# Optimization experiments

Measured on AMD Instinct MI355X. Metric: run time of the kernel, lower is better.

## Reference

```python
import jax, jax.numpy as jnp
import numpy as np

# model dims (DeepSeekV2-Lite-like, reduced expert count)
H = 2048      # hidden_dim
NH = 16       # num_heads
NOPE = 128    # qk_nope_head_dim
ROPE = 64     # qk_rope_head_dim (interleaved rotary)
VD = 128      # v_head_dim
QL = 1536     # q_lora_rank
KVL = 512     # kv_lora_rank
E = 8         # num routed experts
TOPK = 2      # num_experts_per_token
MI = 512      # moe_intermediate_dim
SH_I = 2 * MI # num_shared_experts * moe_intermediate_dim
B = 1
S = 2048
T = B * S
EPS = 1e-6
MOE_SCALE = 1.0  # gating_scaling_factor


def setup_inputs() -> dict:
    key = jax.random.key(0)
    ks = jax.random.split(key, 16)
    def w(k, shape):
        return jax.random.normal(k, shape, dtype=jnp.float32) * 0.02
    # interleaved rotary tables: one angle per (even,odd) pair
    half = ROPE // 2
    pos = jnp.arange(S, dtype=jnp.float32)
    inv_freq = 1.0 / (10000.0 ** (jnp.arange(half, dtype=jnp.float32) * 2.0 / ROPE))
    ang = pos[:, None] * inv_freq[None, :]              # [S, half]
    sin = jnp.tile(jnp.sin(ang), (B, 1))                # [T, half]
    cos = jnp.tile(jnp.cos(ang), (B, 1))
    return {
        "x": jax.random.normal(ks[0], (T, H), jnp.float32),
        "skip": jax.random.normal(ks[1], (T, H), jnp.float32),
        "rotary_sin": sin,
        "rotary_cos": cos,
        "ln1_w": jnp.ones((H,), jnp.float32),
        "ln2_w": jnp.ones((H,), jnp.float32),
        "w_qa": w(ks[2], (QL, H)),
        "qa_norm_w": jnp.ones((QL,), jnp.float32),
        "w_qb": w(ks[3], (NH * (NOPE + ROPE), QL)),
        "w_kva": w(ks[4], (KVL + ROPE, H)),
        "kva_norm_w": jnp.ones((KVL,), jnp.float32),
        "w_kb": w(ks[5], (NH * NOPE, KVL)),
        "w_vb": w(ks[6], (NH * VD, KVL)),
        "w_o": w(ks[7], (H, NH * VD)),
        "gate_w": w(ks[8], (E, H)),
        "moe_up_w": w(ks[9], (E, 2 * MI, H)),
        "moe_down_w": w(ks[10], (E, H, MI)),
        "shared_up_w": w(ks[11], (2 * SH_I, H)),
        "shared_down_w": w(ks[12], (H, SH_I)),
        "batch": B,
    }


def _rms(v, w):
    return v * jax.lax.rsqrt(jnp.mean(v * v, axis=-1, keepdims=True) + EPS) * w


def _rope_interleaved(v, sin, cos):
    # v: [T, nh, ROPE]; sin/cos: [T, ROPE//2]; rotate (even, odd) pairs
    x1, x2 = v[..., 0::2], v[..., 1::2]
    s, c = sin[:, None, :], cos[:, None, :]
    o1 = x1 * c - x2 * s
    o2 = x1 * s + x2 * c
    return jnp.stack([o1, o2], axis=-1).reshape(v.shape)


def reference(x, skip, rotary_sin, rotary_cos, ln1_w, ln2_w, w_qa, qa_norm_w,
              w_qb, w_kva, kva_norm_w, w_kb, w_vb, w_o, gate_w,
              moe_up_w, moe_down_w, shared_up_w, shared_down_w, batch):
    Tt = x.shape[0]
    Sq = Tt // batch
    # SkipRMSNorm #1
    x1 = x + skip
    n1 = _rms(x1, ln1_w)
    # ---- MLA attention (prefill path, decoding_batches=0) ----
    qa = _rms(n1 @ w_qa.T, qa_norm_w)                               # [T, QL]
    q = (qa @ w_qb.T).reshape(Tt, NH, NOPE + ROPE)
    q_nope, q_pe = q[..., :NOPE], q[..., NOPE:]
    q_pe = _rope_interleaved(q_pe, rotary_sin, rotary_cos)
    kv = n1 @ w_kva.T                                               # [T, KVL+ROPE]
    ckv = _rms(kv[:, :KVL], kva_norm_w)
    k_pe = _rope_interleaved(kv[:, KVL:][:, None, :], rotary_sin, rotary_cos)  # [T,1,ROPE]
    k_nope = (ckv @ w_kb.T).reshape(Tt, NH, NOPE)
    v = (ckv @ w_vb.T).reshape(Tt, NH, VD)
    qf = jnp.concatenate([q_nope, q_pe], -1).reshape(batch, Sq, NH, NOPE + ROPE)
    kf = jnp.concatenate([k_nope, jnp.broadcast_to(k_pe, (Tt, NH, ROPE))], -1)
    kf = kf.reshape(batch, Sq, NH, NOPE + ROPE)
    vf = v.reshape(batch, Sq, NH, VD)
    scale = 1.0 / np.sqrt(NOPE + ROPE)
    scores = jnp.einsum('bqhd,bkhd->bhqk', qf, kf) * scale
    causal = jnp.tril(jnp.ones((Sq, Sq), bool))
    scores = jnp.where(causal[None, None], scores, jnp.float32(-1e30))
    p = jax.nn.softmax(scores, axis=-1)
    o = jnp.einsum('bhqk,bkhd->bqhd', p, vf).reshape(Tt, NH * VD)
    attn = o @ w_o.T
    # SkipRMSNorm #2
    x2 = x1 + attn
    n2 = _rms(x2, ln2_w)
    # ---- MoE FFN: softmax gate, greedy top-k, normalized probs ----
    probs = jax.nn.softmax(n2 @ gate_w.T, axis=-1)                  # [T, E]
    tv, ti = jax.lax.top_k(probs, TOPK)
    tv = tv / jnp.sum(tv, axis=-1, keepdims=True) * MOE_SCALE
    routed = jnp.zeros_like(n2)
    for e in range(E):  # fixed small expert count; masked dense dispatch
        we = jnp.sum(tv * (ti == e), axis=-1)                       # [T]
        h = n2 @ moe_up_w[e].T                                      # [T, 2*MI]
        h = jax.nn.silu(h[:, :MI]) * h[:, MI:]
        routed = routed + we[:, None] * (h @ moe_down_w[e].T)
    # shared experts (dense swiglu MLP)
    hs = n2 @ shared_up_w.T
    hs = jax.nn.silu(hs[:, :SH_I]) * hs[:, SH_I:]
    ffn = routed + hs @ shared_down_w.T
    return (x2, ffn)
```

## Files before the change

### kernel.cpp

```cpp
#include <hip/hip_runtime.h>
#include <hip/hip_bf16.h>

#define H 2048
#define NH 16
#define NOPE 128
#define ROPE_D 64
#define DQK 192
#define VD 128
#define QL 1536
#define KVL 512
#define NE 8
#define MI_D 512
#define SHI 1024
#define EPS 1e-6f
#define MAXA 5120

typedef unsigned short bfu;
typedef short bf16x8 __attribute__((ext_vector_type(8)));
typedef float f32x4 __attribute__((ext_vector_type(4)));

#define MFMA16(a, b, c) __builtin_amdgcn_mfma_f32_16x16x32_bf16(a, b, c, 0, 0, 0)

#define BAR_PLAIN()   asm volatile("s_barrier" ::: "memory")
#define BAR_LGKM0()   asm volatile("s_waitcnt lgkmcnt(0)\n\ts_barrier" ::: "memory")
#define BAR_VM4()     asm volatile("s_waitcnt vmcnt(4)\n\ts_barrier" ::: "memory")
#define BAR_VM0()     asm volatile("s_waitcnt vmcnt(0)\n\ts_barrier" ::: "memory")

__device__ __forceinline__ float bf2f(bfu u) {
    union { unsigned int i; float f; } w; w.i = ((unsigned int)u) << 16; return w.f;
}
__device__ __forceinline__ bfu f2bf(float f) {
    union { float f; unsigned int i; } u; u.f = f;
    return (bfu)((u.i + 0x7fffu + ((u.i >> 16) & 1u)) >> 16);
}

__device__ __forceinline__ void async16(const bfu* g, bfu* l) {
    __builtin_amdgcn_global_load_lds((const __attribute__((address_space(1))) void*)g,
                                     (__attribute__((address_space(3))) void*)l, 16, 0, 0);
}

__device__ __forceinline__ float blk_sum(float v) {
    __shared__ float sb[4];
    for (int o = 32; o > 0; o >>= 1) v += __shfl_down(v, o, 64);
    int lane = threadIdx.x & 63, w = threadIdx.x >> 6;
    __syncthreads();
    if (lane == 0) sb[w] = v;
    __syncthreads();
    return sb[0] + sb[1] + sb[2] + sb[3];
}

struct GemmSeg {
    const bfu* A; const bfu* B; void* C; void* C2;
    const int* aidx; const int* eid;
    long bstride;
    int N, K, ldm3, mode, nx, ntiles;
};

__device__ __forceinline__ void gemm_body(const bfu* __restrict__ A, const bfu* __restrict__ B,
                                          void* __restrict__ Cv, void* __restrict__ Cv2,
                                          int N, int K, int ldm3, int mode,
                                          const int* __restrict__ aidx,
                                          const int* __restrict__ eid, long bstride,
                                          int bx, int by,
                                          bfu* sAb, bfu* sBb) {
    bfu (*sA)[128 * 32] = (bfu (*)[128 * 32])sAb;
    bfu (*sB)[128 * 32] = (bfu (*)[128 * 32])sBb;
    const int tid = threadIdx.x;
    const int lane = tid & 63, w = tid >> 6;
    const int quad = lane >> 4, li = lane & 15;
    const int m0 = by * 128, n0 = bx * 128;
    const bfu* Bp = B + (eid ? (size_t)eid[by] * bstride : 0);

    const int l4 = lane >> 2;
    const int lg = lane & 3;
    const int kc = lg ^ ((lane >> 3) & 3);
    int r0 = m0 + w * 32 + l4, r1 = r0 + 16;
    if (aidx) { r0 = aidx[r0]; r1 = aidx[r1]; }
    const bfu* gA0 = A + (size_t)r0 * K + kc * 8;
    const bfu* gA1 = A + (size_t)r1 * K + kc * 8;
    const bfu* gB0 = Bp + (size_t)(n0 + w * 32 + l4) * K + kc * 8;
    const bfu* gB1 = gB0 + (size_t)16 * K;
    const int oA0 = (w * 32) * 32, oA1 = (w * 32 + 16) * 32;

    const int wm = (w >> 1) * 64, wn = (w & 1) * 64;
    const int fg = (quad ^ ((li >> 1) & 3)) * 8;
    int oa[4], ob[4];
#pragma unroll
    for (int t4 = 0; t4 < 4; ++t4) {
        oa[t4] = (wm + t4 * 16 + li) * 32 + fg;
        ob[t4] = (wn + t4 * 16 + li) * 32 + fg;
    }
    f32x4 acc[4][4];
#pragma unroll
    for (int i = 0; i < 4; ++i)
#pragma unroll
        for (int j = 0; j < 4; ++j) acc[i][j] = (f32x4){0.f, 0.f, 0.f, 0.f};

    const int nb = K / 32;
    async16(gA0, &sA[0][oA0]); async16(gA1, &sA[0][oA1]);
    async16(gB0, &sB[0][oA0]); async16(gB1, &sB[0][oA1]);
    async16(gA0 + 32, &sA[1][oA0]); async16(gA1 + 32, &sA[1][oA1]);
    async16(gB0 + 32, &sB[1][oA0]); async16(gB1 + 32, &sB[1][oA1]);

    int cur = 0;
    for (int it = 0; it < nb; ++it) {
        if (it < nb - 1) { BAR_VM4(); } else { BAR_VM0(); }
        bf16x8 av[4], bv[4];
#pragma unroll
        for (int t4 = 0; t4 < 4; ++t4) av[t4] = *(const bf16x8*)&sA[cur][oa[t4]];
#pragma unroll
        for (int t4 = 0; t4 < 4; ++t4) bv[t4] = *(const bf16x8*)&sB[cur][ob[t4]];
        if (it + 2 < nb) {
            const int k1 = (it + 2) * 32;
            int nxt = cur + 2; if (nxt >= 3) nxt -= 3;
            async16(gA0 + k1, &sA[nxt][oA0]); async16(gA1 + k1, &sA[nxt][oA1]);
            async16(gB0 + k1, &sB[nxt][oA0]); async16(gB1 + k1, &sB[nxt][oA1]);
        }
#pragma unroll
        for (int mt = 0; mt < 4; ++mt)
#pragma unroll
            for (int nt = 0; nt < 4; ++nt)
                acc[mt][nt] = MFMA16(av[mt], bv[nt], acc[mt][nt]);
        if (++cur >= 3) cur = 0;
    }

#pragma unroll
    for (int mt = 0; mt < 4; ++mt)
#pragma unroll
        for (int nt = 0; nt < 4; ++nt) {
            int row = m0 + wm + mt * 16 + quad * 4;
            int col = n0 + wn + nt * 16 + li;
            if (mode == 0) {
                float* C = (float*)Cv;
#pragma unroll
                for (int r = 0; r < 4; ++r) C[(size_t)(row + r) * N + col] = acc[mt][nt][r];
            } else if (mode == 1) {
                bfu* C = (bfu*)Cv;
#pragma unroll
                for (int r = 0; r < 4; ++r) C[(size_t)(row + r) * N + col] = f2bf(acc[mt][nt][r]);
            } else {
                if (n0 < 2048) {
                    bfu* C = (bfu*)Cv;
#pragma unroll
                    for (int r = 0; r < 4; ++r) C[(size_t)(row + r) * 2048 + col] = f2bf(acc[mt][nt][r]);
                } else {
                    bfu* C2 = (bfu*)Cv2;
                    ushort4 u;
                    u.x = f2bf(acc[mt][nt][0]); u.y = f2bf(acc[mt][nt][1]);
                    u.z = f2bf(acc[mt][nt][2]); u.w = f2bf(acc[mt][nt][3]);
                    *(ushort4*)(C2 + (size_t)(col - 2048) * ldm3 + row) = u;
                }
            }
        }
}

__global__ __launch_bounds__(256) void gemm_multi(GemmSeg s0, GemmSeg s1) {
    __shared__ bfu sA[3][128 * 32];
    __shared__ bfu sB[3][128 * 32];
    int b = blockIdx.x;
    if (b < s0.ntiles) {
        gemm_body(s0.A, s0.B, s0.C, s0.C2, s0.N, s0.K, s0.ldm3, s0.mode,
                  s0.aidx, s0.eid, s0.bstride, b % s0.nx, b / s0.nx, &sA[0][0], &sB[0][0]);
    } else {
        int lb = b - s0.ntiles;
        gemm_body(s1.A, s1.B, s1.C, s1.C2, s1.N, s1.K, s1.ldm3, s1.mode,
                  s1.aidx, s1.eid, s1.bstride, lb % s1.nx, lb / s1.nx, &sA[0][0], &sB[0][0]);
    }
}

struct CastArgs {
    const float* s[10];
    bfu* d[10];
    unsigned start[11];
    int pad[10];
};
__global__ __launch_bounds__(256) void k_cast_all(CastArgs a) {
    unsigned g = blockIdx.x * 256 + threadIdx.x;
    if (g >= a.start[10]) return;
    int id = 0;
#pragma unroll
    for (int i = 1; i < 10; ++i) if (g >= a.start[i]) id = i;
    size_t i8 = (size_t)(g - a.start[id]) * 8;
    ushort4 u0 = {0, 0, 0, 0}, u1 = {0, 0, 0, 0};
    if (!a.pad[id] || (i8 >> 11) < 576) {
        const float* s = a.s[id];
        float4 x0 = *(const float4*)(s + i8);
        float4 x1 = *(const float4*)(s + i8 + 4);
        u0.x = f2bf(x0.x); u0.y = f2bf(x0.y); u0.z = f2bf(x0.z); u0.w = f2bf(x0.w);
        u1.x = f2bf(x1.x); u1.y = f2bf(x1.y); u1.z = f2bf(x1.z); u1.w = f2bf(x1.w);
    }
    bfu* d = a.d[id];
    *(ushort4*)(d + i8) = u0;
    *(ushort4*)(d + i8 + 4) = u1;
}

__global__ __launch_bounds__(256) void k_add_rms(const float* __restrict__ x, const float* __restrict__ skip,
                                                 const float* __restrict__ w,
                                                 float* __restrict__ x1, bfu* __restrict__ n1b) {
    int t = blockIdx.x;
    size_t base = (size_t)t * H;
    float loc[8]; float ss = 0.f;
#pragma unroll
    for (int i = 0; i < 8; ++i) {
        int c = threadIdx.x + i * 256;
        float v = x[base + c] + skip[base + c];
        loc[i] = v; ss += v * v;
        x1[base + c] = v;
    }
    float tot = blk_sum(ss);
    float r = rsqrtf(tot / (float)H + EPS);
#pragma unroll
    for (int i = 0; i < 8; ++i) {
        int c = threadIdx.x + i * 256;
        n1b[base + c] = f2bf(loc[i] * r * w[c]);
    }
}

__global__ __launch_bounds__(256) void k_qkv_post(const bfu* __restrict__ qkv,
                                                  const float* __restrict__ qa_nw,
                                                  const float* __restrict__ kva_nw,
                                                  const float* __restrict__ sin_, const float* __restrict__ cos_,
                                                  bfu* __restrict__ qab, bfu* __restrict__ ckv,
                                                  bfu* __restrict__ kpe) {
    int t = blockIdx.x;
    const bfu* row = qkv + (size_t)t * 2176;
    float qa[6]; float ss1 = 0.f;
#pragma unroll
    for (int i = 0; i < 6; ++i) {
        float v = bf2f(row[threadIdx.x + i * 256]); qa[i] = v; ss1 += v * v;
    }
    float v0 = bf2f(row[1536 + threadIdx.x]), v1 = bf2f(row[1792 + threadIdx.x]);
    float s1 = blk_sum(ss1);
    float s2 = blk_sum(v0 * v0 + v1 * v1);
    float r1 = rsqrtf(s1 / (float)QL + EPS);
    float r2 = rsqrtf(s2 / 512.f + EPS);
#pragma unroll
    for (int i = 0; i < 6; ++i) {
        int c = threadIdx.x + i * 256;
        qab[(size_t)t * QL + c] = f2bf(qa[i] * r1 * qa_nw[c]);
    }
    ckv[(size_t)t * 512 + threadIdx.x]       = f2bf(v0 * r2 * kva_nw[threadIdx.x]);
    ckv[(size_t)t * 512 + threadIdx.x + 256] = f2bf(v1 * r2 * kva_nw[threadIdx.x + 256]);
    if (threadIdx.x < 32) {
        int p = threadIdx.x;
        float x1v = bf2f(row[2048 + 2 * p]), x2v = bf2f(row[2048 + 2 * p + 1]);
        float s = sin_[t * 32 + p], c = cos_[t * 32 + p];
        kpe[(size_t)t * 64 + 2 * p]     = f2bf(x1v * c - x2v * s);
        kpe[(size_t)t * 64 + 2 * p + 1] = f2bf(x1v * s + x2v * c);
    }
}

__global__ __launch_bounds__(128) void k_flash_mfma(const bfu* __restrict__ qb,
                                                    const bfu* __restrict__ kn,
                                                    const bfu* __restrict__ kpe,
                                                    const bfu* __restrict__ vt,
                                                    bfu* __restrict__ O,
                                                    const float* __restrict__ rsin,
                                                    const float* __restrict__ rcos, int T) {
    __shared__ bfu Ks[32 * 200];
    __shared__ bfu VtL[128 * 32];
    __shared__ bfu P[32 * 40];
    const int tid = threadIdx.x;
    const int lane = tid & 63, w = tid >> 6;
    const int quad = lane >> 4, li = lane & 15;
    const int q0 = ((int)gridDim.x - 1 - (int)blockIdx.x) * 32;
    const int h = blockIdx.y;
    const float scale = 0.07216878364870322f;

    bf16x8 qf[6];
    {
        int qrow = q0 + w * 16 + li;
        const bfu* qp = qb + ((size_t)qrow * NH + h) * DQK;
#pragma unroll
        for (int s6 = 0; s6 < 6; ++s6) {
            bf16x8 v = *(const bf16x8*)(qp + s6 * 32 + quad * 8);
            if (s6 >= 4) {
                int pb = (s6 - 4) * 16 + quad * 4;
#pragma unroll
                for (int j = 0; j < 4; ++j) {
                    float x1 = bf2f((bfu)v[2 * j]), x2 = bf2f((bfu)v[2 * j + 1]);
                    float s = rsin[qrow * 32 + pb + j], c = rcos[qrow * 32 + pb + j];
                    v[2 * j]     = (short)f2bf(x1 * c - x2 * s);
                    v[2 * j + 1] = (short)f2bf(x1 * s + x2 * c);
                }
            }
            qf[s6] = v;
        }
    }
    f32x4 accO[8];
#pragma unroll
    for (int i = 0; i < 8; ++i) accO[i] = (f32x4){0.f, 0.f, 0.f, 0.f};
    float lrow[4] = {0.f, 0.f, 0.f, 0.f};

    int kr[6], kg[6];
#pragma unroll
    for (int it = 0; it < 6; ++it) { int G = tid + it * 128; kr[it] = G / 24; kg[it] = G % 24; }
    int vn[4], vgl[4], vkc[4];
#pragma unroll
    for (int it = 0; it < 4; ++it) {
        int idx = tid + it * 128; vn[it] = idx >> 2; vgl[it] = idx & 3;
        vkc[it] = vgl[it] ^ ((vn[it] >> 1) & 3);
    }
    bf16x8 kreg[6], vreg[4];
#pragma unroll
    for (int it = 0; it < 6; ++it)
        kreg[it] = (kg[it] < 16) ? *(const bf16x8*)(kn + (size_t)kr[it] * (NH * 128) + h * 128 + kg[it] * 8)
                                 : *(const bf16x8*)(kpe + (size_t)kr[it] * 64 + (kg[it] - 16) * 8);
#pragma unroll
    for (int it = 0; it < 4; ++it)
        vreg[it] = *(const bf16x8*)(vt + (size_t)(h * 128 + vn[it]) * T + vkc[it] * 8);

    const int fgv = (quad ^ ((li >> 1) & 3)) * 8;
    const int kend = q0 + 32;
    for (int k0 = 0; k0 < kend; k0 += 32) {
        BAR_PLAIN();
#pragma unroll
        for (int it = 0; it < 6; ++it) *(bf16x8*)(Ks + kr[it] * 200 + kg[it] * 8) = kreg[it];
#pragma unroll
        for (int it = 0; it < 4; ++it) *(bf16x8*)(VtL + vn[it] * 32 + vgl[it] * 8) = vreg[it];
        if (k0 + 32 < kend) {
            int k1 = k0 + 32;
#pragma unroll
            for (int it = 0; it < 6; ++it)
                kreg[it] = (kg[it] < 16) ? *(const bf16x8*)(kn + (size_t)(k1 + kr[it]) * (NH * 128) + h * 128 + kg[it] * 8)
                                         : *(const bf16x8*)(kpe + (size_t)(k1 + kr[it]) * 64 + (kg[it] - 16) * 8);
#pragma unroll
            for (int it = 0; it < 4; ++it)
                vreg[it] = *(const bf16x8*)(vt + (size_t)(h * 128 + vn[it]) * T + k1 + vkc[it] * 8);
        }
        BAR_LGKM0();
        f32x4 s[2];
#pragma unroll
        for (int ct = 0; ct < 2; ++ct) {
            f32x4 a = (f32x4){0.f, 0.f, 0.f, 0.f};
#pragma unroll
            for (int s6 = 0; s6 < 6; ++s6) {
                bf16x8 kf = *(const bf16x8*)(Ks + (ct * 16 + li) * 200 + s6 * 32 + quad * 8);
                a = MFMA16(qf[s6], kf, a);
            }
            s[ct] = a;
        }
#pragma unroll
        for (int r = 0; r < 4; ++r) {
            int row = q0 + w * 16 + quad * 4 + r;
            float p0 = (k0 + li <= row) ? __expf(s[0][r] * scale) : 0.f;
            float p1 = (k0 + 16 + li <= row) ? __expf(s[1][r] * scale) : 0.f;
            s[0][r] = p0; s[1][r] = p1;
            lrow[r] += p0 + p1;
        }
#pragma unroll
        for (int ct = 0; ct < 2; ++ct)
#pragma unroll
            for (int r = 0; r < 4; ++r)
                P[(w * 16 + quad * 4 + r) * 40 + ct * 16 + li] = f2bf(s[ct][r]);
        bf16x8 pf = *(const bf16x8*)(P + (w * 16 + li) * 40 + quad * 8);
#pragma unroll
        for (int v8 = 0; v8 < 8; ++v8) {
            bf16x8 vf = *(const bf16x8*)(VtL + (v8 * 16 + li) * 32 + fgv);
            accO[v8] = MFMA16(pf, vf, accO[v8]);
        }
    }
#pragma unroll
    for (int r = 0; r < 4; ++r) {
        float l = lrow[r];
        l += __shfl_xor(l, 1); l += __shfl_xor(l, 2);
        l += __shfl_xor(l, 4); l += __shfl_xor(l, 8);
        lrow[r] = 1.0f / l;
    }
#pragma unroll
    for (int v8 = 0; v8 < 8; ++v8)
#pragma unroll
        for (int r = 0; r < 4; ++r) {
            float val = accO[v8][r] * lrow[r];
            O[(size_t)(q0 + w * 16 + quad * 4 + r) * (NH * 128) + h * 128 + v8 * 16 + li] = f2bf(val);
        }
}

__global__ __launch_bounds__(256) void k_x2_n2(const float* __restrict__ x1, const bfu* __restrict__ attn,
                                               const float* __restrict__ ln2w, float* __restrict__ outx2,
                                               bfu* __restrict__ n2b, const float* __restrict__ gw,
                                               int* __restrict__ eidx, float* __restrict__ wts,
                                               int* __restrict__ cnt) {
    int t = blockIdx.x;
    size_t base = (size_t)t * H;
    float loc[8]; float ss = 0.f;
#pragma unroll
    for (int i = 0; i < 8; ++i) {
        int c = threadIdx.x + i * 256;
        float vv = x1[base + c] + bf2f(attn[base + c]);
        loc[i] = vv; ss += vv * vv;
        outx2[base + c] = vv;
    }
    float tot = blk_sum(ss);
    float r = rsqrtf(tot / (float)H + EPS);
    float pe[NE] = {0.f, 0.f, 0.f, 0.f, 0.f, 0.f, 0.f, 0.f};
#pragma unroll
    for (int i = 0; i < 8; ++i) {
        int c = threadIdx.x + i * 256;
        float nv = loc[i] * r * ln2w[c];
        n2b[base + c] = f2bf(nv);
#pragma unroll
        for (int e = 0; e < NE; ++e) pe[e] += nv * gw[e * H + c];
    }
    __shared__ float logits[NE];
    for (int e = 0; e < NE; ++e) {
        float tt = blk_sum(pe[e]);
        if (threadIdx.x == 0) logits[e] = tt;
    }
    __syncthreads();
    if (threadIdx.x == 0) {
        float m = logits[0];
        for (int e = 1; e < NE; ++e) m = fmaxf(m, logits[e]);
        float p[NE];
        for (int e = 0; e < NE; ++e) p[e] = __expf(logits[e] - m);
        int i1 = 0;
        for (int e = 1; e < NE; ++e) if (p[e] > p[i1]) i1 = e;
        int i2 = -1;
        for (int e = 0; e < NE; ++e) if (e != i1 && (i2 < 0 || p[e] > p[i2])) i2 = e;
        float denom = p[i1] + p[i2];
        eidx[t * 2] = i1; eidx[t * 2 + 1] = i2;
        wts[t * 2] = p[i1] / denom; wts[t * 2 + 1] = p[i2] / denom;
        atomicAdd(&cnt[i1], 1); atomicAdd(&cnt[i2], 1);
    }
}

__global__ __launch_bounds__(256) void k_moe_init(int* __restrict__ cnt, int* __restrict__ slot,
                                                  int* __restrict__ eid, int* __restrict__ idx,
                                                  float* __restrict__ aw) {
    int tid = threadIdx.x;
    if (tid < NE) { cnt[tid] = 0; slot[tid] = 0; }
    if (tid < 40) eid[tid] = 0;
    for (int i = tid; i < MAXA; i += 256) { idx[i] = 0; aw[i] = 0.f; }
}

__global__ __launch_bounds__(64) void k_moe_scan(const int* __restrict__ cnt, int* __restrict__ base,
                                                 int* __restrict__ eid) {
    if (threadIdx.x == 0) {
        int off = 0;
        for (int e = 0; e < NE; ++e) {
            base[e] = off;
            int nb = (cnt[e] + 127) >> 7;
            for (int j = 0; j < nb; ++j) eid[(off >> 7) + j] = e;
            off += nb << 7;
        }
    }
}

__global__ __launch_bounds__(256) void k_moe_scatter(const int* __restrict__ eidx, const float* __restrict__ wts,
                                                     const int* __restrict__ base, int* __restrict__ slot,
                                                     int* __restrict__ idx, float* __restrict__ aw,
                                                     int* __restrict__ posmap) {
    int t = blockIdx.x * 256 + threadIdx.x;
#pragma unroll
    for (int j = 0; j < 2; ++j) {
        int e = eidx[t * 2 + j];
        int p = base[e] + atomicAdd(&slot[e], 1);
        idx[p] = t; aw[p] = wts[t * 2 + j]; posmap[t * 2 + j] = p;
    }
}

__global__ __launch_bounds__(256) void k_silu_both(const bfu* __restrict__ hsh, bfu* __restrict__ gsh,
                                                   const bfu* __restrict__ hsp, const float* __restrict__ aw,
                                                   bfu* __restrict__ gsp, int T) {
    int b = blockIdx.x;
    if (b < T) {
        const bfu* row = hsh + (size_t)b * 2048;
        bfu* grow = gsh + (size_t)b * 1024;
#pragma unroll
        for (int j = 0; j < 4; ++j) {
            int i = threadIdx.x + j * 256;
            float a = bf2f(row[i]), bb = bf2f(row[1024 + i]);
            grow[i] = f2bf(a / (1.0f + __expf(-a)) * bb);
        }
    } else {
        int row = b - T;
        float we = aw[row];
        const bfu* hr = hsp + (size_t)row * 1024;
        bfu* gr = gsp + (size_t)row * 512;
#pragma unroll
        for (int j = 0; j < 2; ++j) {
            int i = threadIdx.x + j * 256;
            float a = bf2f(hr[i]), bb = bf2f(hr[512 + i]);
            gr[i] = f2bf(we * a / (1.0f + __expf(-a)) * bb);
        }
    }
}

__global__ __launch_bounds__(256) void k_ffn_out(const float* __restrict__ routed, const bfu* __restrict__ dsp,
                                                 const int* __restrict__ posmap, float* __restrict__ out,
                                                 size_t TH) {
    int t = blockIdx.x;
    int p1 = posmap[t * 2], p2 = posmap[t * 2 + 1];
    const bfu* d1 = dsp + (size_t)p1 * H;
    const bfu* d2 = dsp + (size_t)p2 * H;
#pragma unroll
    for (int j = 0; j < 8; ++j) {
        int c = threadIdx.x + j * 256;
        out[TH + (size_t)t * H + c] = routed[(size_t)t * H + c] + bf2f(d1[c]) + bf2f(d2[c]);
    }
}

static inline GemmSeg mk_seg(const bfu* A, const bfu* B, void* C, void* C2,
                             const int* aidx, const int* eid, long bstride,
                             int N, int K, int ldm3, int mode, int nx, int ny) {
    GemmSeg s;
    s.A = A; s.B = B; s.C = C; s.C2 = C2; s.aidx = aidx; s.eid = eid; s.bstride = bstride;
    s.N = N; s.K = K; s.ldm3 = ldm3; s.mode = mode; s.nx = nx; s.ntiles = nx * ny;
    return s;
}

extern "C" void kernel_launch(void* const* d_in, const int* in_sizes, int n_in,
                              void* d_out, int out_size, void* d_ws, size_t ws_size,
                              hipStream_t stream) {
    const float* x      = (const float*)d_in[0];
    const float* skip   = (const float*)d_in[1];
    const float* rsin   = (const float*)d_in[2];
    const float* rcos   = (const float*)d_in[3];
    const float* ln1w   = (const float*)d_in[4];
    const float* ln2w   = (const float*)d_in[5];
    const float* w_qa   = (const float*)d_in[6];
    const float* qa_nw  = (const float*)d_in[7];
    const float* w_qb   = (const float*)d_in[8];
    const float* w_kva  = (const float*)d_in[9];
    const float* kva_nw = (const float*)d_in[10];
    const float* w_kb   = (const float*)d_in[11];
    const float* w_vb   = (const float*)d_in[12];
    const float* w_o    = (const float*)d_in[13];
    const float* gate_w = (const float*)d_in[14];
    const float* mup    = (const float*)d_in[15];
    const float* mdown  = (const float*)d_in[16];
    const float* shup   = (const float*)d_in[17];
    const float* shdown = (const float*)d_in[18];

    const int T = in_sizes[0] / H;

    bfu* WB = (bfu*)d_ws;
    bfu* wqkv_b  = WB + 0;
    bfu* wkbv_b  = WB + 4456448;
    bfu* wqb_b   = WB + 6553600;
    bfu* wo_b    = WB + 11272192;
    bfu* mup_b   = WB + 15466496;
    bfu* mdown_b = WB + 32243712;
    bfu* shup_b  = WB + 40632320;
    bfu* shdn_b  = WB + 44826624;
    const size_t WBYTES = 93847552;

    char* AB = (char*)d_ws + WBYTES;
    float* x1f    = (float*)(AB + 0);
    float* routed = (float*)(AB + 0);
    bfu*   n1b    = (bfu*)(AB + 16777216);
    bfu*   qkvb   = (bfu*)(AB + 25165824);
    bfu*   knb    = (bfu*)(AB + 25165824);
    bfu*   hsp    = (bfu*)(AB + 25165824);
    bfu*   qab    = (bfu*)(AB + 35651584);
    bfu*   gsp    = (bfu*)(AB + 35651584);
    bfu*   qbb    = (bfu*)(AB + 41943040);
    bfu*   attnb  = (bfu*)(AB + 41943040);
    bfu*   ckvb   = (bfu*)(AB + 54525952);
    bfu*   kpeb   = (bfu*)(AB + 56623104);
    char*  G      = AB + 56885248;
    int*   eidx   = (int*)(G);
    float* wts    = (float*)(G + 16384);
    int*   posmap = (int*)(G + 32768);
    int*   midx   = (int*)(G + 49152);
    float* maw    = (float*)(G + 69632);
    int*   mcnt   = (int*)(G + 90112);
    int*   mbase  = (int*)(G + 90112 + 64);
    int*   mslot  = (int*)(G + 90112 + 128);
    int*   meid   = (int*)(G + 90112 + 192);
    bfu*   ob     = (bfu*)(AB + 57016320);
    bfu*   gsb    = (bfu*)(AB + 57016320);
    bfu*   vtb    = (bfu*)(AB + 65404928);
    bfu*   hsb    = (bfu*)(AB + 65404928);
    bfu*   dsp    = (bfu*)(AB + 65404928);
    const size_t REQ = WBYTES + 86376448;
    if (ws_size < REQ) return;

    {
        CastArgs ca;
        const float* ss[10] = {w_qa, w_kva, w_kb, w_vb, w_qb, w_o, mup, mdown, shup, shdown};
        bfu* dd[10] = {wqkv_b, wqkv_b + 3145728, wkbv_b, wkbv_b + 1048576, wqb_b,
                       wo_b, mup_b, mdown_b, shup_b, shdn_b};
        unsigned n8[10] = {393216, 163840, 131072, 131072, 589824, 524288, 2097152, 1048576, 524288, 262144};
        unsigned acc = 0;
        for (int i = 0; i < 10; ++i) { ca.s[i] = ss[i]; ca.d[i] = dd[i]; ca.start[i] = acc; acc += n8[i]; ca.pad[i] = (i == 1); }
        ca.start[10] = acc;
        k_cast_all<<<22912, 256, 0, stream>>>(ca);
    }

    k_add_rms<<<T, 256, 0, stream>>>(x, skip, ln1w, x1f, n1b);
    {
        GemmSeg s = mk_seg(n1b, wqkv_b, qkvb, nullptr, nullptr, nullptr, 0, 2176, H, 0, 1, 2176 / 128, T / 128);
        gemm_multi<<<s.ntiles, 256, 0, stream>>>(s, s);
    }
    k_qkv_post<<<T, 256, 0, stream>>>(qkvb, qa_nw, kva_nw, rsin, rcos, qab, ckvb, kpeb);
    {
        GemmSeg sq = mk_seg(qab, wqb_b, qbb, nullptr, nullptr, nullptr, 0, NH * DQK, QL, 0, 1, (NH * DQK) / 128, T / 128);
        GemmSeg sk = mk_seg(ckvb, wkbv_b, knb, vtb, nullptr, nullptr, 0, 4096, KVL, T, 4, 4096 / 128, T / 128);
        gemm_multi<<<sq.ntiles + sk.ntiles, 256, 0, stream>>>(sq, sk);
    }
    k_flash_mfma<<<dim3(T / 32, NH), 128, 0, stream>>>(qbb, knb, kpeb, vtb, ob, rsin, rcos, T);
    {
        GemmSeg s = mk_seg(ob, wo_b, attnb, nullptr, nullptr, nullptr, 0, H, NH * VD, 0, 1, H / 128, T / 128);
        gemm_multi<<<s.ntiles, 256, 0, stream>>>(s, s);
    }
    k_moe_init<<<1, 256, 0, stream>>>(mcnt, mslot, meid, midx, maw);
    k_x2_n2<<<T, 256, 0, stream>>>(x1f, attnb, ln2w, (float*)d_out, n1b, gate_w, eidx, wts, mcnt);
    k_moe_scan<<<1, 64, 0, stream>>>(mcnt, mbase, meid);
    k_moe_scatter<<<T / 256, 256, 0, stream>>>(eidx, wts, mbase, mslot, midx, maw, posmap);
    {
        GemmSeg ssh = mk_seg(n1b, shup_b, hsb, nullptr, nullptr, nullptr, 0, 2048, H, 0, 1, 2048 / 128, T / 128);
        GemmSeg smo = mk_seg(n1b, mup_b, hsp, nullptr, midx, meid, (long)1024 * H, 1024, H, 0, 1, 1024 / 128, MAXA / 128);
        gemm_multi<<<ssh.ntiles + smo.ntiles, 256, 0, stream>>>(ssh, smo);
    }
    k_silu_both<<<T + MAXA, 256, 0, stream>>>(hsb, gsb, hsp, maw, gsp, T);
    {
        GemmSeg ssd = mk_seg(gsb, shdn_b, routed, nullptr, nullptr, nullptr, 0, H, SHI, 0, 0, H / 128, T / 128);
        GemmSeg smd = mk_seg(gsp, mdown_b, dsp, nullptr, nullptr, meid, (long)H * MI_D, H, MI_D, 0, 1, H / 128, MAXA / 128);
        gemm_multi<<<ssd.ntiles + smd.ntiles, 256, 0, stream>>>(ssd, smd);
    }
    k_ffn_out<<<T, 256, 0, stream>>>(routed, dsp, posmap, (float*)d_out, (size_t)T * H);
}
```

Measured before the change: 650.4 us.

## Enlarge flash attention tiles to 64, widen weight cast, use shuffle gate reduction

The flash attention kernel now handles 64 query rows per block with 4 waves and 64-key tiles. That halves the number of K/V tile loads per query and the barrier count per key, at the cost of more LDS and registers. The weight cast kernel now converts 16 elements per thread instead of 8, cutting thread count and index overhead. The MoE gate logits are reduced with wave shuffles and one shared-memory step, replacing eight block-wide reductions.

```diff
diff --git a/kernel.cpp b/kernel.cpp
--- a/kernel.cpp
+++ b/kernel.cpp
@@ -180,18 +180,19 @@
     int id = 0;
 #pragma unroll
     for (int i = 1; i < 10; ++i) if (g >= a.start[i]) id = i;
-    size_t i8 = (size_t)(g - a.start[id]) * 8;
-    ushort4 u0 = {0, 0, 0, 0}, u1 = {0, 0, 0, 0};
-    if (!a.pad[id] || (i8 >> 11) < 576) {
+    size_t i16 = (size_t)(g - a.start[id]) * 16;
+    ushort4 u[4] = {};
+    if (!a.pad[id] || (i16 >> 11) < 576) {
         const float* s = a.s[id];
-        float4 x0 = *(const float4*)(s + i8);
-        float4 x1 = *(const float4*)(s + i8 + 4);
-        u0.x = f2bf(x0.x); u0.y = f2bf(x0.y); u0.z = f2bf(x0.z); u0.w = f2bf(x0.w);
-        u1.x = f2bf(x1.x); u1.y = f2bf(x1.y); u1.z = f2bf(x1.z); u1.w = f2bf(x1.w);
+#pragma unroll
+        for (int j = 0; j < 4; ++j) {
+            float4 x = *(const float4*)(s + i16 + j * 4);
+            u[j].x = f2bf(x.x); u[j].y = f2bf(x.y); u[j].z = f2bf(x.z); u[j].w = f2bf(x.w);
+        }
     }
     bfu* d = a.d[id];
-    *(ushort4*)(d + i8) = u0;
-    *(ushort4*)(d + i8 + 4) = u1;
+#pragma unroll
+    for (int j = 0; j < 4; ++j) *(ushort4*)(d + i16 + j * 4) = u[j];
 }
 
 __global__ __launch_bounds__(256) void k_add_rms(const float* __restrict__ x, const float* __restrict__ skip,
@@ -250,20 +251,20 @@
     }
 }
 
-__global__ __launch_bounds__(128) void k_flash_mfma(const bfu* __restrict__ qb,
+__global__ __launch_bounds__(256) void k_flash_mfma(const bfu* __restrict__ qb,
                                                     const bfu* __restrict__ kn,
                                                     const bfu* __restrict__ kpe,
                                                     const bfu* __restrict__ vt,
                                                     bfu* __restrict__ O,
                                                     const float* __restrict__ rsin,
                                                     const float* __restrict__ rcos, int T) {
-    __shared__ bfu Ks[32 * 200];
-    __shared__ bfu VtL[128 * 32];
-    __shared__ bfu P[32 * 40];
+    __shared__ bfu Ks[64 * 200];
+    __shared__ bfu VtL[2][128 * 32];
+    __shared__ bfu P[64 * 72];
     const int tid = threadIdx.x;
     const int lane = tid & 63, w = tid >> 6;
     const int quad = lane >> 4, li = lane & 15;
-    const int q0 = ((int)gridDim.x - 1 - (int)blockIdx.x) * 32;
+    const int q0 = ((int)gridDim.x - 1 - (int)blockIdx.x) * 64;
     const int h = blockIdx.y;
     const float scale = 0.07216878364870322f;
 
@@ -294,12 +295,12 @@
 
     int kr[6], kg[6];
 #pragma unroll
-    for (int it = 0; it < 6; ++it) { int G = tid + it * 128; kr[it] = G / 24; kg[it] = G % 24; }
+    for (int it = 0; it < 6; ++it) { int G = tid + it * 256; kr[it] = G / 24; kg[it] = G % 24; }
     int vn[4], vgl[4], vkc[4];
 #pragma unroll
     for (int it = 0; it < 4; ++it) {
-        int idx = tid + it * 128; vn[it] = idx >> 2; vgl[it] = idx & 3;
-        vkc[it] = vgl[it] ^ ((vn[it] >> 1) & 3);
+        int idx = tid + it * 256; vn[it] = idx >> 3; vgl[it] = idx & 7;
+        vkc[it] = (vgl[it] & 4) | ((vgl[it] & 3) ^ ((vn[it] >> 1) & 3));
     }
     bf16x8 kreg[6], vreg[4];
 #pragma unroll
@@ -311,15 +312,16 @@
         vreg[it] = *(const bf16x8*)(vt + (size_t)(h * 128 + vn[it]) * T + vkc[it] * 8);
 
     const int fgv = (quad ^ ((li >> 1) & 3)) * 8;
-    const int kend = q0 + 32;
-    for (int k0 = 0; k0 < kend; k0 += 32) {
+    const int kend = q0 + 64;
+    for (int k0 = 0; k0 < kend; k0 += 64) {
         BAR_PLAIN();
 #pragma unroll
         for (int it = 0; it < 6; ++it) *(bf16x8*)(Ks + kr[it] * 200 + kg[it] * 8) = kreg[it];
 #pragma unroll
-        for (int it = 0; it < 4; ++it) *(bf16x8*)(VtL + vn[it] * 32 + vgl[it] * 8) = vreg[it];
-        if (k0 + 32 < kend) {
-            int k1 = k0 + 32;
+        for (int it = 0; it < 4; ++it)
+            *(bf16x8*)(VtL[vgl[it] >> 2] + vn[it] * 32 + (vgl[it] & 3) * 8) = vreg[it];
+        if (k0 + 64 < kend) {
+            int k1 = k0 + 64;
 #pragma unroll
             for (int it = 0; it < 6; ++it)
                 kreg[it] = (kg[it] < 16) ? *(const bf16x8*)(kn + (size_t)(k1 + kr[it]) * (NH * 128) + h * 128 + kg[it] * 8)
@@ -329,9 +331,9 @@
                 vreg[it] = *(const bf16x8*)(vt + (size_t)(h * 128 + vn[it]) * T + k1 + vkc[it] * 8);
         }
         BAR_LGKM0();
-        f32x4 s[2];
-#pragma unroll
-        for (int ct = 0; ct < 2; ++ct) {
+        f32x4 s[4];
+#pragma unroll
+        for (int ct = 0; ct < 4; ++ct) {
             f32x4 a = (f32x4){0.f, 0.f, 0.f, 0.f};
 #pragma unroll
             for (int s6 = 0; s6 < 6; ++s6) {
@@ -341,24 +343,30 @@
             s[ct] = a;
         }
 #pragma unroll
-        for (int r = 0; r < 4; ++r) {
-            int row = q0 + w * 16 + quad * 4 + r;
-            float p0 = (k0 + li <= row) ? __expf(s[0][r] * scale) : 0.f;
-            float p1 = (k0 + 16 + li <= row) ? __expf(s[1][r] * scale) : 0.f;
-            s[0][r] = p0; s[1][r] = p1;
-            lrow[r] += p0 + p1;
-        }
-#pragma unroll
-        for (int ct = 0; ct < 2; ++ct)
+        for (int ct = 0; ct < 4; ++ct)
+#pragma unroll
+            for (int r = 0; r < 4; ++r) {
+                int row = q0 + w * 16 + quad * 4 + r;
+                float p = (k0 + ct * 16 + li <= row) ? __expf(s[ct][r] * scale) : 0.f;
+                s[ct][r] = p;
+                lrow[r] += p;
+            }
+#pragma unroll
+        for (int ct = 0; ct < 4; ++ct)
 #pragma unroll
             for (int r = 0; r < 4; ++r)
-                P[(w * 16 + quad * 4 + r) * 40 + ct * 16 + li] = f2bf(s[ct][r]);
-        bf16x8 pf = *(const bf16x8*)(P + (w * 16 + li) * 40 + quad * 8);
-#pragma unroll
-        for (int v8 = 0; v8 < 8; ++v8) {
-            bf16x8 vf = *(const bf16x8*)(VtL + (v8 * 16 + li) * 32 + fgv);
-            accO[v8] = MFMA16(pf, vf, accO[v8]);
-        }
+                P[(w * 16 + quad * 4 + r) * 72 + ct * 16 + li] = f2bf(s[ct][r]);
+        bf16x8 pf[2];
+#pragma unroll
+        for (int ks = 0; ks < 2; ++ks)
+            pf[ks] = *(const bf16x8*)(P + (w * 16 + li) * 72 + ks * 32 + quad * 8);
+#pragma unroll
+        for (int v8 = 0; v8 < 8; ++v8)
+#pragma unroll
+            for (int ks = 0; ks < 2; ++ks) {
+                bf16x8 vf = *(const bf16x8*)(VtL[ks] + (v8 * 16 + li) * 32 + fgv);
+                accO[v8] = MFMA16(pf[ks], vf, accO[v8]);
+            }
     }
 #pragma unroll
     for (int r = 0; r < 4; ++r) {
@@ -402,15 +410,22 @@
 #pragma unroll
         for (int e = 0; e < NE; ++e) pe[e] += nv * gw[e * H + c];
     }
-    __shared__ float logits[NE];
+    __shared__ float sred[4][NE];
+    int lane = threadIdx.x & 63, wv = threadIdx.x >> 6;
+#pragma unroll
     for (int e = 0; e < NE; ++e) {
-        float tt = blk_sum(pe[e]);
-        if (threadIdx.x == 0) logits[e] = tt;
+        float v = pe[e];
+        for (int o = 32; o > 0; o >>= 1) v += __shfl_down(v, o, 64);
+        if (lane == 0) sred[wv][e] = v;
     }
     __syncthreads();
     if (threadIdx.x == 0) {
-        float m = logits[0];
-        for (int e = 1; e < NE; ++e) m = fmaxf(m, logits[e]);
+        float logits[NE];
+        float m = -1e30f;
+        for (int e = 0; e < NE; ++e) {
+            logits[e] = sred[0][e] + sred[1][e] + sred[2][e] + sred[3][e];
+            m = fmaxf(m, logits[e]);
+        }
         float p[NE];
         for (int e = 0; e < NE; ++e) p[e] = __expf(logits[e] - m);
         int i1 = 0;
@@ -581,11 +596,11 @@
         const float* ss[10] = {w_qa, w_kva, w_kb, w_vb, w_qb, w_o, mup, mdown, shup, shdown};
         bfu* dd[10] = {wqkv_b, wqkv_b + 3145728, wkbv_b, wkbv_b + 1048576, wqb_b,
                        wo_b, mup_b, mdown_b, shup_b, shdn_b};
-        unsigned n8[10] = {393216, 163840, 131072, 131072, 589824, 524288, 2097152, 1048576, 524288, 262144};
+        unsigned n16[10] = {196608, 81920, 65536, 65536, 294912, 262144, 1048576, 524288, 262144, 131072};
         unsigned acc = 0;
-        for (int i = 0; i < 10; ++i) { ca.s[i] = ss[i]; ca.d[i] = dd[i]; ca.start[i] = acc; acc += n8[i]; ca.pad[i] = (i == 1); }
+        for (int i = 0; i < 10; ++i) { ca.s[i] = ss[i]; ca.d[i] = dd[i]; ca.start[i] = acc; acc += n16[i]; ca.pad[i] = (i == 1); }
         ca.start[10] = acc;
-        k_cast_all<<<22912, 256, 0, stream>>>(ca);
+        k_cast_all<<<(acc + 255) / 256, 256, 0, stream>>>(ca);
     }
 
     k_add_rms<<<T, 256, 0, stream>>>(x, skip, ln1w, x1f, n1b);
@@ -599,7 +614,7 @@
         GemmSeg sk = mk_seg(ckvb, wkbv_b, knb, vtb, nullptr, nullptr, 0, 4096, KVL, T, 4, 4096 / 128, T / 128);
         gemm_multi<<<sq.ntiles + sk.ntiles, 256, 0, stream>>>(sq, sk);
     }
-    k_flash_mfma<<<dim3(T / 32, NH), 128, 0, stream>>>(qbb, knb, kpeb, vtb, ob, rsin, rcos, T);
+    k_flash_mfma<<<dim3(T / 64, NH), 256, 0, stream>>>(qbb, knb, kpeb, vtb, ob, rsin, rcos, T);
     {
         GemmSeg s = mk_seg(ob, wo_b, attnb, nullptr, nullptr, nullptr, 0, H, NH * VD, 0, 1, H / 128, T / 128);
         gemm_multi<<<s.ntiles, 256, 0, stream>>>(s, s);
```

Result: no change. 638.0 us (-1.9%).
